# Kernel optimization log

Hardware: AMD Instinct MI355X
Metric: run time of the kernel (lower is better)

The kernel has to match this reference:

```python
import jax, jax.numpy as jnp
import numpy as np

B, N, F = 512, 64, 64
ROBOT_DIM, HUMAN_DIM, HID = 9, 5, 128
K = 3  # Chebyshev order


def setup_inputs() -> dict:
    key = jax.random.key(0)
    ks = jax.random.split(key, 16)
    # complete directed graph without self loops, shared across the batch
    src, dst = np.nonzero(~np.eye(N, dtype=bool))
    edge_index = jnp.asarray(np.stack([src, dst]), dtype=jnp.int32)  # [2, E]
    s = 0.05
    return {
        "robot_x": jax.random.normal(ks[0], (B, 1, ROBOT_DIM), jnp.float32),
        "human_x": jax.random.normal(ks[1], (B, N - 1, HUMAN_DIM), jnp.float32),
        "edge_index": edge_index,
        "wr1_w": jax.random.normal(ks[2], (ROBOT_DIM, HID), jnp.float32) * s,
        "wr1_b": jax.random.normal(ks[3], (HID,), jnp.float32) * s,
        "wr2_w": jax.random.normal(ks[4], (HID, F), jnp.float32) * s,
        "wr2_b": jax.random.normal(ks[5], (F,), jnp.float32) * s,
        "wh1_w": jax.random.normal(ks[6], (HUMAN_DIM, HID), jnp.float32) * s,
        "wh1_b": jax.random.normal(ks[7], (HID,), jnp.float32) * s,
        "wh2_w": jax.random.normal(ks[8], (HID, F), jnp.float32) * s,
        "wh2_b": jax.random.normal(ks[9], (F,), jnp.float32) * s,
        "cheb_w": jax.random.normal(ks[10], (K, F, F), jnp.float32) * s,
        "cheb_b": jax.random.normal(ks[11], (F,), jnp.float32) * s,
    }


def reference(robot_x, human_x, edge_index, wr1_w, wr1_b, wr2_w, wr2_b,
              wh1_w, wh1_b, wh2_w, wh2_b, cheb_w, cheb_b):
    # MLP embeddings with last_relu=True
    r = jax.nn.relu(robot_x @ wr1_w + wr1_b)
    r = jax.nn.relu(r @ wr2_w + wr2_b)            # [B, 1, F]
    h = jax.nn.relu(human_x @ wh1_w + wh1_b)
    h = jax.nn.relu(h @ wh2_w + wh2_b)            # [B, N-1, F]
    X = jnp.concatenate([r, h], axis=1)           # [B, N, F]

    src, dst = edge_index[0], edge_index[1]
    n = X.shape[1]
    # PyG ChebConv sym-normalized scaled Laplacian with lambda_max=2:
    # L_hat = -D^{-1/2} A D^{-1/2}  (edge weights all ones, no self loops)
    deg = jax.ops.segment_sum(jnp.ones(src.shape[0], X.dtype), src, num_segments=n)
    dinv = jnp.where(deg > 0, deg ** -0.5, 0.0)
    w = -(dinv[src] * dinv[dst])                  # [E]

    def prop(x):  # x: [B, N, F] -> L_hat @ x per batch via gather/scatter
        msg = x[:, src, :] * w[None, :, None]     # [B, E, F]
        return jnp.zeros_like(x).at[:, dst, :].add(msg)

    Tx0 = X
    Tx1 = prop(X)
    Tx2 = 2.0 * prop(Tx1) - Tx0
    Tx = jnp.stack([Tx0, Tx1, Tx2], axis=0)       # [K, B, N, F]
    out = jnp.einsum("kbnf,kfo->bno", Tx, cheb_w) + cheb_b
    return out[:, 0, :]                           # robot node output [B, F]
```

## Files before the change

### kernel.cpp

```cpp
#include <hip/hip_runtime.h>


#define BDIM 256

typedef __attribute__((ext_vector_type(8))) short bf16x8;
typedef __attribute__((ext_vector_type(4))) float f32x4;

static __device__ __forceinline__ unsigned short f2bf(float f) {
    unsigned int u = __float_as_uint(f);
    u += 0x7FFF + ((u >> 16) & 1);
    return (unsigned short)(u >> 16);
}

__global__ __launch_bounds__(256) void dgcrnn_mfma(
    const float* __restrict__ robot_x,
    const float* __restrict__ human_x,
    const float* __restrict__ wr1, const float* __restrict__ wr1_b,
    const float* __restrict__ wr2, const float* __restrict__ wr2_b,
    const float* __restrict__ wh1, const float* __restrict__ wh1_b,
    const float* __restrict__ wh2, const float* __restrict__ wh2_b,
    const float* __restrict__ cw,  const float* __restrict__ cb,
    float* __restrict__ out)
{
    __shared__ float x_lds[324];
    __shared__ float wh1_l[768];
    __shared__ float wr1_l[1280];
    __shared__ float wh2b_l[64];
    __shared__ float rrow[128];
    __shared__ unsigned int wh2T[4096];
    __shared__ short fragA[8192];
    __shared__ float part[256];
    __shared__ float hpart[256];
    __shared__ float r_s[64], s_s[64];

    const int t = threadIdx.x;
    const int b = blockIdx.x;
    const int l = t & 63;
    const int w = t >> 6;

    for (int i = t; i < 324; i += BDIM)
        x_lds[i] = (i < 9) ? robot_x[b * 9 + i] : human_x[b * 315 + (i - 9)];
    for (int i = t; i < 768; i += BDIM)
        wh1_l[i] = (i < 640) ? wh1[i] : wh1_b[i - 640];
    for (int i = t; i < 1280; i += BDIM)
        wr1_l[i] = (i < 1152) ? wr1[i] : wr1_b[i - 1152];
    if (t < 64) wh2b_l[t] = wh2_b[t];
    for (int rr = 0; rr < 16; ++rr) {
        int p  = rr * 256 + t;
        int o  = p & 63, kp = p >> 6;
        float v0 = wh2[(2 * kp) * 64 + o];
        float v1 = wh2[(2 * kp + 1) * 64 + o];
        unsigned int wv = (unsigned int)f2bf(v0) | ((unsigned int)f2bf(v1) << 16);
        wh2T[o * 64 + (kp ^ ((o & 15) << 2))] = wv;
    }
    __syncthreads();

    #pragma unroll
    for (int s = 0; s < 4; ++s) {
        int slot = s * 256 + t;
        int row  = ((slot >> 8) << 4) | (slot & 15);
        int k0   = ((slot >> 6) & 3) * 32 + ((slot >> 4) & 3) * 8;
        bf16x8 v;
        #pragma unroll
        for (int j = 0; j < 8; ++j) v[j] = 0;
        if (row != 63) {
            float a8[8];
            #pragma unroll
            for (int j = 0; j < 8; ++j) a8[j] = wh1_l[640 + k0 + j];
            #pragma unroll
            for (int i = 0; i < 5; ++i) {
                float xv = x_lds[9 + row * 5 + i];
                #pragma unroll
                for (int j = 0; j < 8; ++j)
                    a8[j] = fmaf(xv, wh1_l[i * 128 + k0 + j], a8[j]);
            }
            #pragma unroll
            for (int j = 0; j < 8; ++j) v[j] = (short)f2bf(fmaxf(a8[j], 0.f));
        }
        *reinterpret_cast<bf16x8*>(&fragA[slot * 8]) = v;
    }
    if (t < 128) {
        float a = wr1_l[1152 + t];
        #pragma unroll
        for (int i = 0; i < 9; ++i) a = fmaf(x_lds[i], wr1_l[i * 128 + t], a);
        rrow[t] = fmaxf(a, 0.f);
    }
    __syncthreads();

    {
        int o = t & 63, q = t >> 6;
        float rp = 0.f;
        #pragma unroll
        for (int j = 0; j < 32; ++j) {
            int k = q * 32 + j;
            rp = fmaf(rrow[k], wr2[k * 64 + o], rp);
        }
        part[q * 64 + o] = rp;
    }

    {
        const int c = l & 15, g = l >> 4;
        bf16x8 af[4];
        #pragma unroll
        for (int kt = 0; kt < 4; ++kt)
            af[kt] = *reinterpret_cast<const bf16x8*>(&fragA[((w * 4 + kt) * 64 + l) * 8]);
        #pragma unroll
        for (int nt = 0; nt < 4; ++nt) {
            const int o = nt * 16 + c;
            f32x4 acc = {0.f, 0.f, 0.f, 0.f};
            #pragma unroll
            for (int kt = 0; kt < 4; ++kt) {
                int kw0 = kt * 16 + g * 4;
                bf16x8 bfv = *reinterpret_cast<const bf16x8*>(
                    &wh2T[o * 64 + (kw0 ^ (c << 2))]);
                acc = __builtin_amdgcn_mfma_f32_16x16x32_bf16(af[kt], bfv, acc, 0, 0, 0);
            }
            float bias = wh2b_l[o];
            float s4 = 0.f;
            #pragma unroll
            for (int reg = 0; reg < 4; ++reg) {
                int node = w * 16 + g * 4 + reg;
                float hv = fmaxf(acc[reg] + bias, 0.f);
                s4 += (node == 63) ? 0.f : hv;
            }
            s4 += __shfl_xor(s4, 16, 64);
            s4 += __shfl_xor(s4, 32, 64);
            if (g == 0) hpart[w * 64 + o] = s4;
        }
    }
    __syncthreads();

    if (t < 64) {
        float hs = hpart[t] + hpart[64 + t] + hpart[128 + t] + hpart[192 + t];
        float r  = part[t] + part[64 + t] + part[128 + t] + part[192 + t] + wr2_b[t];
        r = fmaxf(r, 0.f);
        r_s[t] = r;
        s_s[t] = r + hs;
    }
    __syncthreads();

    {
        const float c1 = 1.0f / 63.0f;
        const float c2 = 2.0f / 3969.0f - 1.0f;
        const float c3 = 124.0f / 3969.0f;
        const int o = t & 63, q = t >> 6;
        float a = 0.f;
        #pragma unroll
        for (int j = 0; j < 16; ++j) {
            int f = q * 16 + j;
            float rv = r_s[f], sv = s_s[f];
            float w0 = cw[f * 64 + o];
            float w1 = cw[4096 + f * 64 + o];
            float w2v = cw[8192 + f * 64 + o];
            a += rv * (w0 + c1 * w1 + c2 * w2v) + sv * (c3 * w2v - c1 * w1);
        }
        part[q * 64 + o] = a;
    }
    __syncthreads();
    if (t < 64)
        out[b * 64 + t] = part[t] + part[64 + t] + part[128 + t] + part[192 + t] + cb[t];
}

extern "C" void kernel_launch(void* const* d_in, const int* in_sizes, int n_in,
                              void* d_out, int out_size, void* d_ws, size_t ws_size,
                              hipStream_t stream) {
    const float* robot_x = (const float*)d_in[0];
    const float* human_x = (const float*)d_in[1];
    const float* wr1   = (const float*)d_in[3];
    const float* wr1_b = (const float*)d_in[4];
    const float* wr2   = (const float*)d_in[5];
    const float* wr2_b = (const float*)d_in[6];
    const float* wh1   = (const float*)d_in[7];
    const float* wh1_b = (const float*)d_in[8];
    const float* wh2   = (const float*)d_in[9];
    const float* wh2_b = (const float*)d_in[10];
    const float* cw    = (const float*)d_in[11];
    const float* cb    = (const float*)d_in[12];
    float* out = (float*)d_out;

    dgcrnn_mfma<<<512, BDIM, 0, stream>>>(robot_x, human_x,
                                          wr1, wr1_b, wr2, wr2_b,
                                          wh1, wh1_b, wh2, wh2_b,
                                          cw, cb, out);
}
```

Baseline: 12.68 us.

## Double block size to 512 threads, prefetch weights as float4 into registers

Raises the block to 512 threads and redistributes the work. Each thread owns 4 consecutive output columns and prefetches the wr2 and Chebyshev weights as float4 into registers at kernel entry, so those global loads overlap the LDS staging. The MFMA stage now splits the N tiles across wave pairs, and the wh2 transpose uses vectorized loads. The cost is larger 32-way partial-sum reductions done by 64 threads and higher register pressure under launch_bounds(512,4).

```diff
diff --git a/kernel.cpp b/kernel.cpp
--- a/kernel.cpp
+++ b/kernel.cpp
@@ -1,7 +1,7 @@
 #include <hip/hip_runtime.h>
 
 
-#define BDIM 256
+#define BDIM 512
 
 typedef __attribute__((ext_vector_type(8))) short bf16x8;
 typedef __attribute__((ext_vector_type(4))) float f32x4;
@@ -12,7 +12,7 @@
     return (unsigned short)(u >> 16);
 }
 
-__global__ __launch_bounds__(256) void dgcrnn_mfma(
+__global__ __launch_bounds__(512, 4) void dgcrnn_mfma(
     const float* __restrict__ robot_x,
     const float* __restrict__ human_x,
     const float* __restrict__ wr1, const float* __restrict__ wr1_b,
@@ -27,16 +27,30 @@
     __shared__ float wr1_l[1280];
     __shared__ float wh2b_l[64];
     __shared__ float rrow[128];
-    __shared__ unsigned int wh2T[4096];
-    __shared__ short fragA[8192];
-    __shared__ float part[256];
+    __shared__ __align__(16) unsigned int wh2T[4096];
+    __shared__ __align__(16) short fragA[8192];
+    __shared__ __align__(16) float rp_lds[2048];
     __shared__ float hpart[256];
     __shared__ float r_s[64], s_s[64];
 
-    const int t = threadIdx.x;
-    const int b = blockIdx.x;
-    const int l = t & 63;
-    const int w = t >> 6;
+    const int t   = threadIdx.x;
+    const int b   = blockIdx.x;
+    const int l   = t & 63;
+    const int w   = t >> 6;
+    const int oq  = t & 15;
+    const int o0  = oq * 4;
+    const int g16 = t >> 4;
+
+    float4 wr2q[4];
+    #pragma unroll
+    for (int j = 0; j < 4; ++j)
+        wr2q[j] = *(const float4*)&wr2[(g16 * 4 + j) * 64 + o0];
+    float4 cwq[2][3];
+    #pragma unroll
+    for (int ff = 0; ff < 2; ++ff)
+        #pragma unroll
+        for (int k = 0; k < 3; ++k)
+            cwq[ff][k] = *(const float4*)&cw[k * 4096 + (g16 * 2 + ff) * 64 + o0];
 
     for (int i = t; i < 324; i += BDIM)
         x_lds[i] = (i < 9) ? robot_x[b * 9 + i] : human_x[b * 315 + (i - 9)];
@@ -45,19 +59,24 @@
     for (int i = t; i < 1280; i += BDIM)
         wr1_l[i] = (i < 1152) ? wr1[i] : wr1_b[i - 1152];
     if (t < 64) wh2b_l[t] = wh2_b[t];
-    for (int rr = 0; rr < 16; ++rr) {
-        int p  = rr * 256 + t;
-        int o  = p & 63, kp = p >> 6;
-        float v0 = wh2[(2 * kp) * 64 + o];
-        float v1 = wh2[(2 * kp + 1) * 64 + o];
-        unsigned int wv = (unsigned int)f2bf(v0) | ((unsigned int)f2bf(v1) << 16);
-        wh2T[o * 64 + (kp ^ ((o & 15) << 2))] = wv;
-    }
-    __syncthreads();
-
-    #pragma unroll
-    for (int s = 0; s < 4; ++s) {
-        int slot = s * 256 + t;
+    #pragma unroll
+    for (int kk = 0; kk < 2; ++kk) {
+        int kp = g16 * 2 + kk;
+        float4 e = *(const float4*)&wh2[(2 * kp) * 64 + o0];
+        float4 d = *(const float4*)&wh2[(2 * kp + 1) * 64 + o0];
+        #pragma unroll
+        for (int c = 0; c < 4; ++c) {
+            int o = o0 + c;
+            unsigned int wv = (unsigned int)f2bf((&e.x)[c])
+                            | ((unsigned int)f2bf((&d.x)[c]) << 16);
+            wh2T[o * 64 + (kp ^ ((o & 15) << 2))] = wv;
+        }
+    }
+    __syncthreads();
+
+    #pragma unroll
+    for (int s = 0; s < 2; ++s) {
+        int slot = s * 512 + t;
         int row  = ((slot >> 8) << 4) | (slot & 15);
         int k0   = ((slot >> 6) & 3) * 32 + ((slot >> 4) & 3) * 8;
         bf16x8 v;
@@ -88,25 +107,29 @@
     __syncthreads();
 
     {
-        int o = t & 63, q = t >> 6;
-        float rp = 0.f;
-        #pragma unroll
-        for (int j = 0; j < 32; ++j) {
-            int k = q * 32 + j;
-            rp = fmaf(rrow[k], wr2[k * 64 + o], rp);
-        }
-        part[q * 64 + o] = rp;
+        float4 rp = {0.f, 0.f, 0.f, 0.f};
+        #pragma unroll
+        for (int j = 0; j < 4; ++j) {
+            float hv = rrow[g16 * 4 + j];
+            rp.x = fmaf(hv, wr2q[j].x, rp.x);
+            rp.y = fmaf(hv, wr2q[j].y, rp.y);
+            rp.z = fmaf(hv, wr2q[j].z, rp.z);
+            rp.w = fmaf(hv, wr2q[j].w, rp.w);
+        }
+        *(float4*)&rp_lds[g16 * 64 + o0] = rp;
     }
 
     {
         const int c = l & 15, g = l >> 4;
+        const int mt = w >> 1;
         bf16x8 af[4];
         #pragma unroll
         for (int kt = 0; kt < 4; ++kt)
-            af[kt] = *reinterpret_cast<const bf16x8*>(&fragA[((w * 4 + kt) * 64 + l) * 8]);
-        #pragma unroll
-        for (int nt = 0; nt < 4; ++nt) {
-            const int o = nt * 16 + c;
+            af[kt] = *reinterpret_cast<const bf16x8*>(&fragA[((mt * 4 + kt) * 64 + l) * 8]);
+        #pragma unroll
+        for (int ni = 0; ni < 2; ++ni) {
+            const int nt = (w & 1) * 2 + ni;
+            const int o  = nt * 16 + c;
             f32x4 acc = {0.f, 0.f, 0.f, 0.f};
             #pragma unroll
             for (int kt = 0; kt < 4; ++kt) {
@@ -119,21 +142,23 @@
             float s4 = 0.f;
             #pragma unroll
             for (int reg = 0; reg < 4; ++reg) {
-                int node = w * 16 + g * 4 + reg;
+                int node = mt * 16 + g * 4 + reg;
                 float hv = fmaxf(acc[reg] + bias, 0.f);
                 s4 += (node == 63) ? 0.f : hv;
             }
             s4 += __shfl_xor(s4, 16, 64);
             s4 += __shfl_xor(s4, 32, 64);
-            if (g == 0) hpart[w * 64 + o] = s4;
+            if (g == 0) hpart[mt * 64 + o] = s4;
         }
     }
     __syncthreads();
 
     if (t < 64) {
         float hs = hpart[t] + hpart[64 + t] + hpart[128 + t] + hpart[192 + t];
-        float r  = part[t] + part[64 + t] + part[128 + t] + part[192 + t] + wr2_b[t];
-        r = fmaxf(r, 0.f);
+        float rsum = wr2_b[t];
+        #pragma unroll
+        for (int kg = 0; kg < 32; ++kg) rsum += rp_lds[kg * 64 + t];
+        float r = fmaxf(rsum, 0.f);
         r_s[t] = r;
         s_s[t] = r + hs;
     }
@@ -143,22 +168,29 @@
         const float c1 = 1.0f / 63.0f;
         const float c2 = 2.0f / 3969.0f - 1.0f;
         const float c3 = 124.0f / 3969.0f;
-        const int o = t & 63, q = t >> 6;
-        float a = 0.f;
-        #pragma unroll
-        for (int j = 0; j < 16; ++j) {
-            int f = q * 16 + j;
+        float4 a4 = {0.f, 0.f, 0.f, 0.f};
+        #pragma unroll
+        for (int ff = 0; ff < 2; ++ff) {
+            int f = g16 * 2 + ff;
             float rv = r_s[f], sv = s_s[f];
-            float w0 = cw[f * 64 + o];
-            float w1 = cw[4096 + f * 64 + o];
-            float w2v = cw[8192 + f * 64 + o];
-            a += rv * (w0 + c1 * w1 + c2 * w2v) + sv * (c3 * w2v - c1 * w1);
-        }
-        part[q * 64 + o] = a;
-    }
-    __syncthreads();
-    if (t < 64)
-        out[b * 64 + t] = part[t] + part[64 + t] + part[128 + t] + part[192 + t] + cb[t];
+            #pragma unroll
+            for (int c = 0; c < 4; ++c) {
+                float w0  = (&cwq[ff][0].x)[c];
+                float w1  = (&cwq[ff][1].x)[c];
+                float w2v = (&cwq[ff][2].x)[c];
+                (&a4.x)[c] += rv * (w0 + c1 * w1 + c2 * w2v)
+                            + sv * (c3 * w2v - c1 * w1);
+            }
+        }
+        *(float4*)&rp_lds[g16 * 64 + o0] = a4;
+    }
+    __syncthreads();
+    if (t < 64) {
+        float a = cb[t];
+        #pragma unroll
+        for (int kg = 0; kg < 32; ++kg) a += rp_lds[kg * 64 + t];
+        out[b * 64 + t] = a;
+    }
 }
 
 extern "C" void kernel_launch(void* const* d_in, const int* in_sizes, int n_in,
```

New measurement: 12.42 us. 2.0% less time.
